# Optimization experiments

Measured on AMD Instinct MI355X. Metric: run time of the kernel, lower is better.

The kernel has to match this reference:

```python
import jax, jax.numpy as jnp
import numpy as np


def setup_inputs() -> dict:
    key = jax.random.key(0)
    kx, kc = jax.random.split(key)
    N, K, D = 32768, 4096, 512
    x = jax.random.normal(kx, (N, D), dtype=jnp.float32)
    # matches torch.rand(K, D) * 0.2 - 0.1
    codebook = jax.random.uniform(kc, (K, D), dtype=jnp.float32) * 0.2 - 0.1
    return {"x": x, "codebook": codebook}


def reference(x, codebook):
    x_sq = jnp.sum(x * x, axis=-1, keepdims=True)            # [N, 1]
    c_sq = jnp.sum(codebook * codebook, axis=-1)             # [K]
    dists = x_sq - 2.0 * jnp.einsum('nd,kd->nk', x, codebook) + c_sq[None, :]
    Z = jnp.argmin(dists, axis=-1)                           # [N] int
    q = codebook[Z]                                          # [N, D] gather
    q_with_st = x + jax.lax.stop_gradient(q - x)             # straight-through
    vq_loss = jnp.mean((jax.lax.stop_gradient(q) - x) ** 2)
    commitment_loss = jnp.mean((jax.lax.stop_gradient(x) - q) ** 2)
    return Z, q_with_st, vq_loss, commitment_loss
```

## Files before the change

kernel.cpp:

```cpp
#include <hip/hip_runtime.h>

static constexpr int N = 32768;
static constexpr int K = 4096;
static constexpr int D = 512;

typedef _Float16 f16x8 __attribute__((ext_vector_type(8)));
typedef float f32x4 __attribute__((ext_vector_type(4)));

#define GLD16(GP, LP)                                                   \
  __builtin_amdgcn_global_load_lds(                                     \
      (const __attribute__((address_space(1))) void*)(GP),              \
      (__attribute__((address_space(3))) void*)(LP), 16, 0, 0)

__global__ __launch_bounds__(256) void rowsq_convert_kernel(
    const float* __restrict__ in, float* __restrict__ sqout,
    _Float16* __restrict__ hi, float scale, int rows) {
  __shared__ float ls[8][512];
  int rb = blockIdx.x * 8;
  int tid = threadIdx.x;
#pragma unroll
  for (int g2 = 0; g2 < 2; ++g2) {
    int g = g2 * 256 + tid;
    int r = g >> 6;
    int c8 = (g & 63) * 8;
    const float4* p = (const float4*)(in + (size_t)(rb + r) * D + c8);
    float4 a = p[0], b = p[1];
    float s[8] = {a.x, a.y, a.z, a.w, b.x, b.y, b.z, b.w};
    union { _Float16 h[8]; f16x8 v; } H;
#pragma unroll
    for (int jj = 0; jj < 8; ++jj) {
      H.h[jj] = (_Float16)(s[jj] * scale);
      ls[r][c8 + jj] = s[jj];
    }
    *(f16x8*)(hi + (size_t)(rb + r) * D + c8) = H.v;
  }
  __syncthreads();
  int rr = tid >> 5;
  int l = tid & 31;
  const float* p = &ls[rr][(l >> 3) * 128 + (l & 7)];
  float r = 0.f;
#pragma unroll
  for (int i = 0; i < 16; ++i) {
    float v = p[i * 8];
    r = __fadd_rn(r, __fmul_rn(v, v));
  }
  r = __fadd_rn(r, __shfl_xor(r, 1));
  r = __fadd_rn(r, __shfl_xor(r, 2));
  r = __fadd_rn(r, __shfl_xor(r, 4));
  r = __fadd_rn(r, __shfl_xor(r, 8));
  r = __fadd_rn(r, __shfl_xor(r, 16));
  if (l == 0) sqout[rb + rr] = r;
}

__global__ __launch_bounds__(256) void transpose_kernel(
    const float* __restrict__ in, float* __restrict__ outT) {
  __shared__ float t[32][33];
  int bk = blockIdx.x;
  int bd = blockIdx.y;
  int tx = threadIdx.x, ty = threadIdx.y;
#pragma unroll
  for (int j = 0; j < 32; j += 8)
    t[ty + j][tx] = in[(size_t)(bk * 32 + ty + j) * D + bd * 32 + tx];
  __syncthreads();
#pragma unroll
  for (int j = 0; j < 32; j += 8)
    outT[(size_t)(bd * 32 + ty + j) * K + bk * 32 + tx] = t[tx][ty + j];
}

__global__ __launch_bounds__(256) void mfma_argmin_kernel(
    const _Float16* __restrict__ xh, const _Float16* __restrict__ ch,
    const float* __restrict__ xsq, const float* __restrict__ csq,
    float* __restrict__ pv1, int* __restrict__ pi1, float* __restrict__ pv2) {
  __shared__ __align__(16) _Float16 Ah[2][128 * 32];
  __shared__ __align__(16) _Float16 Bh[2][128 * 32];
  __shared__ float mbv1[128];
  __shared__ int mbi1[128];
  __shared__ float mbv2[128];

  int bid = blockIdx.x;
  int xcd = bid & 7, j = bid >> 3;
  int sup = j >> 6, win = j & 63;
  int rowPanel = xcd * 32 + (sup >> 2) * 8 + (win >> 3);
  int colPanel = (sup & 3) * 8 + (win & 7);

  int tid = threadIdx.x;
  int w = tid >> 6, l = tid & 63;
  int wr = w >> 1, wc = w & 1;
  int wrow = wr * 64, wcol = wc * 64;
  int rA = l & 15, g = l >> 4;

  const size_t rowBase = (size_t)rowPanel * 128;
  const size_t colBase = (size_t)colPanel * 128;

  f32x4 acc[4][4];
#pragma unroll
  for (int mi = 0; mi < 4; ++mi)
#pragma unroll
    for (int ni = 0; ni < 4; ++ni) acc[mi][ni] = (f32x4)0.f;

  const int r0 = tid >> 2, s0 = tid & 3;
  const int cs = s0 ^ ((r0 >> 1) & 3);
  const int swz = (g ^ ((rA >> 1) & 3)) * 8;

  const _Float16* aSrc = xh + (rowBase + r0) * D + cs * 8;
  const _Float16* bSrc = ch + (colBase + r0) * D + cs * 8;

  auto stage = [&](int buf, int kt) {
    const int dOff = kt * 32;
    GLD16(aSrc + dOff, &Ah[buf][(size_t)tid * 8]);
    GLD16(aSrc + dOff + (size_t)64 * D, &Ah[buf][(size_t)(tid + 256) * 8]);
    GLD16(bSrc + dOff, &Bh[buf][(size_t)tid * 8]);
    GLD16(bSrc + dOff + (size_t)64 * D, &Bh[buf][(size_t)(tid + 256) * 8]);
  };

  stage(0, 0);
  int cur = 0;
  for (int kt = 0; kt < 16; ++kt) {
    __syncthreads();
    if (kt < 15) stage(cur ^ 1, kt + 1);

    f16x8 ah[4], bh[4];
#pragma unroll
    for (int f = 0; f < 4; ++f) {
      ah[f] = *(const f16x8*)&Ah[cur][(wrow + f * 16 + rA) * 32 + swz];
      bh[f] = *(const f16x8*)&Bh[cur][(wcol + f * 16 + rA) * 32 + swz];
    }
#pragma unroll
    for (int mi = 0; mi < 4; ++mi)
#pragma unroll
      for (int ni = 0; ni < 4; ++ni)
        acc[mi][ni] =
            __builtin_amdgcn_mfma_f32_16x16x32_f16(ah[mi], bh[ni], acc[mi][ni], 0, 0, 0);
    cur ^= 1;
  }

  const float inv2048 = 1.0f / 2048.0f;
  float fv1[4][4], fv2[4][4];
  int fi1[4][4];
#pragma unroll
  for (int mi = 0; mi < 4; ++mi) {
#pragma unroll
    for (int r = 0; r < 4; ++r) {
      int row_l = wrow + mi * 16 + g * 4 + r;
      float xq = xsq[rowBase + row_l];
      float bv1 = 1e30f, bv2 = 1e30f;
      int bi1 = 0x7fffffff;
#pragma unroll
      for (int ni = 0; ni < 4; ++ni) {
        int col = (int)colBase + wcol + ni * 16 + rA;
        float S = acc[mi][ni][r];
        float dsc = (xq - S * inv2048) + csq[col];
        if (dsc < bv1 || (dsc == bv1 && col < bi1)) {
          bv2 = bv1; bv1 = dsc; bi1 = col;
        } else if (dsc < bv2) {
          bv2 = dsc;
        }
      }
#pragma unroll
      for (int m = 1; m < 16; m <<= 1) {
        float ov1 = __shfl_xor(bv1, m);
        int oi1 = __shfl_xor(bi1, m);
        float ov2 = __shfl_xor(bv2, m);
        if (ov1 < bv1 || (ov1 == bv1 && oi1 < bi1)) {
          bv2 = fminf(bv1, ov2); bv1 = ov1; bi1 = oi1;
        } else {
          bv2 = fminf(bv2, ov1);
        }
      }
      fv1[mi][r] = bv1; fv2[mi][r] = bv2; fi1[mi][r] = bi1;
      if (wc == 1 && rA == 0) {
        mbv1[row_l] = bv1; mbi1[row_l] = bi1; mbv2[row_l] = bv2;
      }
    }
  }
  __syncthreads();
  if (wc == 0 && rA == 0) {
#pragma unroll
    for (int mi = 0; mi < 4; ++mi) {
#pragma unroll
      for (int r = 0; r < 4; ++r) {
        int row_l = wrow + mi * 16 + g * 4 + r;
        float bv1 = fv1[mi][r], bv2 = fv2[mi][r];
        int bi1 = fi1[mi][r];
        float ov1 = mbv1[row_l];
        int oi1 = mbi1[row_l];
        float ov2 = mbv2[row_l];
        if (ov1 < bv1 || (ov1 == bv1 && oi1 < bi1)) {
          bv2 = fminf(bv1, ov2); bv1 = ov1; bi1 = oi1;
        } else {
          bv2 = fminf(bv2, ov1);
        }
        size_t o = (size_t)colPanel * N + (rowBase + row_l);
        pv1[o] = bv1; pi1[o] = bi1; pv2[o] = bv2;
      }
    }
  }
}

__global__ __launch_bounds__(256) void reduce_kernel(
    const float* __restrict__ pv1, const int* __restrict__ pi1,
    const float* __restrict__ pv2, float* __restrict__ zout,
    int* __restrict__ ctr, int* __restrict__ list, float eps) {
  int row = blockIdx.x * 256 + threadIdx.x;
  if (row >= N) return;
  float v1 = 1e30f, v2 = 1e30f;
  int i1 = 0x7fffffff;
  for (int jj = 0; jj < 32; ++jj) {
    float ov1 = pv1[(size_t)jj * N + row];
    float ov2 = pv2[(size_t)jj * N + row];
    int oi1 = pi1[(size_t)jj * N + row];
    if (ov1 < v1 || (ov1 == v1 && oi1 < i1)) {
      v2 = fminf(v1, ov2); v1 = ov1; i1 = oi1;
    } else {
      v2 = fminf(v2, ov1);
    }
  }
  zout[row] = (float)i1;
  if (v2 - v1 < eps) {
    int p = atomicAdd(ctr, 1);
    if (p < N) list[p] = row;
  }
}

static constexpr int RT_ROWS = 16;
static constexpr int RT_PANELS = 8;
static constexpr int CHUNK_D = 8;

__global__ __launch_bounds__(256) void rescore_tiled_kernel(
    const float* __restrict__ x, const float* __restrict__ cbT,
    const float* __restrict__ xsq, const float* __restrict__ csq,
    const int* __restrict__ ctr, const int* __restrict__ list,
    float* __restrict__ prv, int* __restrict__ pri) {
  __shared__ float xs[RT_ROWS][D + 4];
  __shared__ __align__(16) float cbs[2][CHUNK_D][512];
  int cnt = *ctr;
  if (cnt > N) cnt = N;
  int nTiles = (cnt + RT_ROWS - 1) / RT_ROWS;
  int nItems = nTiles * RT_PANELS;
  int tid = threadIdx.x;
  int ty = tid >> 4;
  int tx = tid & 15;

  for (int item = blockIdx.x; item < nItems; item += gridDim.x) {
    int tileIdx = item >> 3;
    int panel = item & 7;
    int base = tileIdx * RT_ROWS;
    int colPanel = panel * 512;
    __syncthreads();

    for (int i = tid; i < RT_ROWS * (D / 4); i += 256) {
      int r = i >> 7;
      int d4 = i & 127;
      int fi = base + r;
      int row = list[fi < cnt ? fi : 0];
      ((float4*)&xs[r][0])[d4] = ((const float4*)(x + (size_t)row * D))[d4];
    }

    auto stageCb = [&](int buf, int chk) {
      const float* src = cbT + (size_t)(chk * CHUNK_D) * K + colPanel;
#pragma unroll
      for (int it = 0; it < 4; ++it) {
        int f = it * 256 + tid;
        int dd = f >> 7, c4 = f & 127;
        GLD16(src + (size_t)dd * K + c4 * 4, &cbs[buf][0][0] + (size_t)f * 4);
      }
    };

    stageCb(0, 0);
    float acc[32];
#pragma unroll
    for (int c = 0; c < 32; ++c) acc[c] = 0.f;

    int cur = 0;
    for (int chk = 0; chk < D / CHUNK_D; ++chk) {
      __syncthreads();
      if (chk < D / CHUNK_D - 1) stageCb(cur ^ 1, chk + 1);
#pragma unroll
      for (int dd = 0; dd < CHUNK_D; ++dd) {
        float xa = xs[ty][chk * CHUNK_D + dd];
        const float4* cp = (const float4*)&cbs[cur][dd][0];
#pragma unroll
        for (int jj = 0; jj < 8; ++jj) {
          float4 v = cp[tx + jj * 16];
          acc[jj * 4 + 0] = fmaf(xa, v.x, acc[jj * 4 + 0]);
          acc[jj * 4 + 1] = fmaf(xa, v.y, acc[jj * 4 + 1]);
          acc[jj * 4 + 2] = fmaf(xa, v.z, acc[jj * 4 + 2]);
          acc[jj * 4 + 3] = fmaf(xa, v.w, acc[jj * 4 + 3]);
        }
      }
      cur ^= 1;
    }

    int fi = base + ty;
    int row = list[fi < cnt ? fi : 0];
    float xq = xsq[row];
    float bv = 1e30f;
    int bi = 0x7fffffff;
#pragma unroll
    for (int jj = 0; jj < 8; ++jj) {
#pragma unroll
      for (int q = 0; q < 4; ++q) {
        int col = colPanel + jj * 64 + tx * 4 + q;
        float a = acc[jj * 4 + q];
        float two = __fadd_rn(a, a);
        float t = __fsub_rn(xq, two);
        float dsc = __fadd_rn(t, csq[col]);
        if (dsc < bv || (dsc == bv && col < bi)) { bv = dsc; bi = col; }
      }
    }
#pragma unroll
    for (int m = 1; m < 16; m <<= 1) {
      float ov = __shfl_xor(bv, m);
      int oi = __shfl_xor(bi, m);
      if (ov < bv || (ov == bv && oi < bi)) { bv = ov; bi = oi; }
    }
    if (tx == 0 && fi < cnt) {
      prv[(size_t)fi * RT_PANELS + panel] = bv;
      pri[(size_t)fi * RT_PANELS + panel] = bi;
    }
  }
}

__global__ __launch_bounds__(256) void rescore_reduce_kernel(
    const float* __restrict__ prv, const int* __restrict__ pri,
    const int* __restrict__ ctr, const int* __restrict__ list,
    float* __restrict__ zout) {
  int cnt = *ctr;
  if (cnt > N) cnt = N;
  for (int fi = blockIdx.x * 256 + threadIdx.x; fi < cnt;
       fi += gridDim.x * 256) {
    float bv = 1e30f;
    int bi = 0x7fffffff;
#pragma unroll
    for (int p = 0; p < RT_PANELS; ++p) {
      float v = prv[(size_t)fi * RT_PANELS + p];
      int i = pri[(size_t)fi * RT_PANELS + p];
      if (v < bv || (v == bv && i < bi)) { bv = v; bi = i; }
    }
    zout[list[fi]] = (float)bi;
  }
}

static constexpr int BM = 64;
static constexpr int BKc = 128;
static constexpr int BD = 32;

__global__ __launch_bounds__(256) void argmin_fp32_kernel(
    const float* __restrict__ x, const float* __restrict__ cb,
    const float* __restrict__ xsq, const float* __restrict__ csq,
    float* __restrict__ zout) {
  __shared__ float xs[BD][BM];
  __shared__ float cs_[BD][BKc];
  __shared__ float mv[BM][16];
  __shared__ int mi[BM][16];

  int tid = threadIdx.x;
  int tx = tid & 15;
  int ty = tid >> 4;
  int row0 = blockIdx.x * BM;

  float bestv[4];
  int besti[4];
  float xsqr[4];
#pragma unroll
  for (int i = 0; i < 4; ++i) {
    bestv[i] = 3.4e38f;
    besti[i] = 0x7fffffff;
    xsqr[i] = xsq[row0 + ty * 4 + i];
  }

  for (int kt = 0; kt < K; kt += BKc) {
    float acc[4][8];
#pragma unroll
    for (int i = 0; i < 4; ++i)
#pragma unroll
      for (int jj = 0; jj < 8; ++jj) acc[i][jj] = 0.f;

    for (int dt = 0; dt < D; dt += BD) {
      __syncthreads();
      {
        int r = tid >> 2, d0 = (tid & 3) * 8;
        const float* src = x + (size_t)(row0 + r) * D + dt + d0;
        float4 v0 = *(const float4*)(src);
        float4 v1 = *(const float4*)(src + 4);
        xs[d0 + 0][r] = v0.x; xs[d0 + 1][r] = v0.y;
        xs[d0 + 2][r] = v0.z; xs[d0 + 3][r] = v0.w;
        xs[d0 + 4][r] = v1.x; xs[d0 + 5][r] = v1.y;
        xs[d0 + 6][r] = v1.z; xs[d0 + 7][r] = v1.w;
      }
      {
        int kk = tid >> 1, d0 = (tid & 1) * 16;
        const float* src = cb + (size_t)(kt + kk) * D + dt + d0;
        float4 v0 = *(const float4*)(src);
        float4 v1 = *(const float4*)(src + 4);
        float4 v2 = *(const float4*)(src + 8);
        float4 v3 = *(const float4*)(src + 12);
        cs_[d0 + 0][kk] = v0.x;  cs_[d0 + 1][kk] = v0.y;
        cs_[d0 + 2][kk] = v0.z;  cs_[d0 + 3][kk] = v0.w;
        cs_[d0 + 4][kk] = v1.x;  cs_[d0 + 5][kk] = v1.y;
        cs_[d0 + 6][kk] = v1.z;  cs_[d0 + 7][kk] = v1.w;
        cs_[d0 + 8][kk] = v2.x;  cs_[d0 + 9][kk] = v2.y;
        cs_[d0 + 10][kk] = v2.z; cs_[d0 + 11][kk] = v2.w;
        cs_[d0 + 12][kk] = v3.x; cs_[d0 + 13][kk] = v3.y;
        cs_[d0 + 14][kk] = v3.z; cs_[d0 + 15][kk] = v3.w;
      }
      __syncthreads();
#pragma unroll 4
      for (int d = 0; d < BD; ++d) {
        float xa[4], cv[8];
        *(float4*)&xa[0] = *(const float4*)&xs[d][ty * 4];
        *(float4*)&cv[0] = *(const float4*)&cs_[d][tx * 8];
        *(float4*)&cv[4] = *(const float4*)&cs_[d][tx * 8 + 4];
#pragma unroll
        for (int i = 0; i < 4; ++i)
#pragma unroll
          for (int jj = 0; jj < 8; ++jj)
            acc[i][jj] = fmaf(xa[i], cv[jj], acc[i][jj]);
      }
    }

#pragma unroll
    for (int jj = 0; jj < 8; ++jj) {
      int k = kt + tx * 8 + jj;
      float cq = csq[k];
#pragma unroll
      for (int i = 0; i < 4; ++i) {
        float two = __fadd_rn(acc[i][jj], acc[i][jj]);
        float t = __fsub_rn(xsqr[i], two);
        float dsc = __fadd_rn(t, cq);
        if (dsc < bestv[i]) { bestv[i] = dsc; besti[i] = k; }
      }
    }
  }

  __syncthreads();
#pragma unroll
  for (int i = 0; i < 4; ++i) {
    mv[ty * 4 + i][tx] = bestv[i];
    mi[ty * 4 + i][tx] = besti[i];
  }
  __syncthreads();
  if (tid < BM) {
    float bv = mv[tid][0];
    int bi = mi[tid][0];
#pragma unroll
    for (int t = 1; t < 16; ++t) {
      float v = mv[tid][t];
      int ii = mi[tid][t];
      if (v < bv || (v == bv && ii < bi)) { bv = v; bi = ii; }
    }
    zout[row0 + tid] = (float)bi;
  }
}

__global__ __launch_bounds__(256) void gather_kernel(
    const float* __restrict__ x, const float* __restrict__ cb,
    const float* __restrict__ zf, float* __restrict__ qout,
    float* __restrict__ partial) {
  __shared__ float red[256];
  const size_t TOT4 = (size_t)N * D / 4;
  size_t t0 = (size_t)blockIdx.x * 256 + threadIdx.x;
  float lsum = 0.f;
  for (size_t f = t0; f < TOT4; f += (size_t)2048 * 256) {
    int n = (int)(f >> 7);
    int d4 = (int)(f & 127);
    int z = (int)zf[n];
    float4 xv = ((const float4*)x)[f];
    float4 qv = *(const float4*)(cb + (size_t)z * D + d4 * 4);
    float dx0 = __fsub_rn(qv.x, xv.x);
    float dx1 = __fsub_rn(qv.y, xv.y);
    float dx2 = __fsub_rn(qv.z, xv.z);
    float dx3 = __fsub_rn(qv.w, xv.w);
    float4 o;
    o.x = __fadd_rn(xv.x, dx0);
    o.y = __fadd_rn(xv.y, dx1);
    o.z = __fadd_rn(xv.z, dx2);
    o.w = __fadd_rn(xv.w, dx3);
    ((float4*)qout)[f] = o;
    lsum += dx0 * dx0 + dx1 * dx1 + dx2 * dx2 + dx3 * dx3;
  }
  red[threadIdx.x] = lsum;
  __syncthreads();
  for (int s = 128; s > 0; s >>= 1) {
    if (threadIdx.x < s) red[threadIdx.x] += red[threadIdx.x + s];
    __syncthreads();
  }
  if (threadIdx.x == 0) partial[blockIdx.x] = red[0];
}

__global__ __launch_bounds__(256) void loss_kernel(const float* __restrict__ partial,
                                                   float* __restrict__ loss_out) {
  __shared__ float red[256];
  float s = 0.f;
  for (int i = threadIdx.x; i < 2048; i += 256) s += partial[i];
  red[threadIdx.x] = s;
  __syncthreads();
  for (int k = 128; k > 0; k >>= 1) {
    if (threadIdx.x < k) red[threadIdx.x] += red[threadIdx.x + k];
    __syncthreads();
  }
  if (threadIdx.x == 0) {
    float m = red[0] / (float)((size_t)N * D);
    loss_out[0] = m;
    loss_out[1] = m;
  }
}

static constexpr size_t OFF_XSQ = 0;
static constexpr size_t OFF_CSQ = 131072;
static constexpr size_t OFF_PART = 147456;
static constexpr size_t OFF_CTR = 155648;
static constexpr size_t OFF_LIST = 155904;
static constexpr size_t OFF_PV1 = 286976;
static constexpr size_t OFF_PI1 = OFF_PV1 + 4194304;
static constexpr size_t OFF_PV2 = OFF_PI1 + 4194304;
static constexpr size_t OFF_PRV = OFF_PV2 + 4194304;
static constexpr size_t OFF_PRI = OFF_PRV + 1048576;
static constexpr size_t WS_REQ = OFF_PRI + 1048576;

extern "C" void kernel_launch(void* const* d_in, const int* in_sizes, int n_in,
                              void* d_out, int out_size, void* d_ws, size_t ws_size,
                              hipStream_t stream) {
  const float* x = (const float*)d_in[0];
  const float* cb = (const float*)d_in[1];
  float* out = (float*)d_out;

  float* zout = out;
  float* qout = out + N;
  float* lout = out + N + (size_t)N * D;

  char* ws = (char*)d_ws;
  float* xsq = (float*)(ws + OFF_XSQ);
  float* csq = (float*)(ws + OFF_CSQ);
  float* partial = (float*)(ws + OFF_PART);

  _Float16* xhi = (_Float16*)qout;
  float* cbT = (float*)((char*)qout + (size_t)N * D * 2);
  _Float16* chi = (_Float16*)((char*)cbT + (size_t)D * K * 4);

  rowsq_convert_kernel<<<dim3(N / 8), dim3(256), 0, stream>>>(x, xsq, xhi,
                                                              16.0f, N);
  rowsq_convert_kernel<<<dim3(K / 8), dim3(256), 0, stream>>>(cb, csq, chi,
                                                              256.0f, K);

  if (ws_size >= WS_REQ) {
    int* ctr = (int*)(ws + OFF_CTR);
    int* list = (int*)(ws + OFF_LIST);
    float* pv1 = (float*)(ws + OFF_PV1);
    int* pi1 = (int*)(ws + OFF_PI1);
    float* pv2 = (float*)(ws + OFF_PV2);
    float* prv = (float*)(ws + OFF_PRV);
    int* pri = (int*)(ws + OFF_PRI);

    transpose_kernel<<<dim3(K / 32, D / 32), dim3(32, 8), 0, stream>>>(cb, cbT);
    hipMemsetAsync(ctr, 0, sizeof(int), stream);
    mfma_argmin_kernel<<<dim3((N / 128) * (K / 128)), dim3(256), 0, stream>>>(
        xhi, chi, xsq, csq, pv1, pi1, pv2);
    reduce_kernel<<<dim3(N / 256), dim3(256), 0, stream>>>(pv1, pi1, pv2, zout,
                                                           ctr, list, 0.02f);
    rescore_tiled_kernel<<<dim3(1024), dim3(256), 0, stream>>>(
        x, cbT, xsq, csq, ctr, list, prv, pri);
    rescore_reduce_kernel<<<dim3(128), dim3(256), 0, stream>>>(prv, pri, ctr,
                                                               list, zout);
  } else {
    argmin_fp32_kernel<<<dim3(N / BM), dim3(256), 0, stream>>>(x, cb, xsq, csq,
                                                               zout);
  }

  gather_kernel<<<dim3(2048), dim3(256), 0, stream>>>(x, cb, zout, qout, partial);
  loss_kernel<<<dim3(1), dim3(256), 0, stream>>>(partial, lout);
}
```

Baseline: 537.6 us.

## Widen MFMA argmin tile to 128x256 with per-wave full-row coverage

The fp16 MFMA distance/argmin kernel now computes a 128x256 tile per block instead of 128x128, so each wave covers all 128 rows against its own 64 columns with an 8x4 accumulator array. This halves the number of column panels, which halves the partial-result buffers and the reduce loop, and raises data reuse per LDS load. The cost is more accumulator registers (launch bounds set to 2 blocks/SM), larger LDS for B, and a four-way cross-wave merge through shared memory.

```diff
diff --git a/kernel.cpp b/kernel.cpp
--- a/kernel.cpp
+++ b/kernel.cpp
@@ -67,34 +67,33 @@
     outT[(size_t)(bd * 32 + ty + j) * K + bk * 32 + tx] = t[tx][ty + j];
 }
 
-__global__ __launch_bounds__(256) void mfma_argmin_kernel(
+__global__ __launch_bounds__(256, 2) void mfma_argmin_kernel(
     const _Float16* __restrict__ xh, const _Float16* __restrict__ ch,
     const float* __restrict__ xsq, const float* __restrict__ csq,
     float* __restrict__ pv1, int* __restrict__ pi1, float* __restrict__ pv2) {
   __shared__ __align__(16) _Float16 Ah[2][128 * 32];
-  __shared__ __align__(16) _Float16 Bh[2][128 * 32];
-  __shared__ float mbv1[128];
-  __shared__ int mbi1[128];
-  __shared__ float mbv2[128];
+  __shared__ __align__(16) _Float16 Bh[2][256 * 32];
+  __shared__ float mbv1[128][4];
+  __shared__ float mbv2[128][4];
+  __shared__ int mbi1[128][4];
 
   int bid = blockIdx.x;
   int xcd = bid & 7, j = bid >> 3;
   int sup = j >> 6, win = j & 63;
-  int rowPanel = xcd * 32 + (sup >> 2) * 8 + (win >> 3);
-  int colPanel = (sup & 3) * 8 + (win & 7);
+  int rowPanel = xcd * 32 + (sup >> 1) * 8 + (win >> 3);
+  int colPanel = (sup & 1) * 8 + (win & 7);
 
   int tid = threadIdx.x;
   int w = tid >> 6, l = tid & 63;
-  int wr = w >> 1, wc = w & 1;
-  int wrow = wr * 64, wcol = wc * 64;
+  int wcol = w * 64;
   int rA = l & 15, g = l >> 4;
 
   const size_t rowBase = (size_t)rowPanel * 128;
-  const size_t colBase = (size_t)colPanel * 128;
-
-  f32x4 acc[4][4];
-#pragma unroll
-  for (int mi = 0; mi < 4; ++mi)
+  const size_t colBase = (size_t)colPanel * 256;
+
+  f32x4 acc[8][4];
+#pragma unroll
+  for (int mi = 0; mi < 8; ++mi)
 #pragma unroll
     for (int ni = 0; ni < 4; ++ni) acc[mi][ni] = (f32x4)0.f;
 
@@ -111,6 +110,8 @@
     GLD16(aSrc + dOff + (size_t)64 * D, &Ah[buf][(size_t)(tid + 256) * 8]);
     GLD16(bSrc + dOff, &Bh[buf][(size_t)tid * 8]);
     GLD16(bSrc + dOff + (size_t)64 * D, &Bh[buf][(size_t)(tid + 256) * 8]);
+    GLD16(bSrc + dOff + (size_t)128 * D, &Bh[buf][(size_t)(tid + 512) * 8]);
+    GLD16(bSrc + dOff + (size_t)192 * D, &Bh[buf][(size_t)(tid + 768) * 8]);
   };
 
   stage(0, 0);
@@ -119,14 +120,15 @@
     __syncthreads();
     if (kt < 15) stage(cur ^ 1, kt + 1);
 
-    f16x8 ah[4], bh[4];
-#pragma unroll
-    for (int f = 0; f < 4; ++f) {
-      ah[f] = *(const f16x8*)&Ah[cur][(wrow + f * 16 + rA) * 32 + swz];
+    f16x8 bh[4], ah[8];
+#pragma unroll
+    for (int f = 0; f < 4; ++f)
       bh[f] = *(const f16x8*)&Bh[cur][(wcol + f * 16 + rA) * 32 + swz];
-    }
-#pragma unroll
-    for (int mi = 0; mi < 4; ++mi)
+#pragma unroll
+    for (int f = 0; f < 8; ++f)
+      ah[f] = *(const f16x8*)&Ah[cur][(f * 16 + rA) * 32 + swz];
+#pragma unroll
+    for (int mi = 0; mi < 8; ++mi)
 #pragma unroll
       for (int ni = 0; ni < 4; ++ni)
         acc[mi][ni] =
@@ -135,13 +137,11 @@
   }
 
   const float inv2048 = 1.0f / 2048.0f;
-  float fv1[4][4], fv2[4][4];
-  int fi1[4][4];
-#pragma unroll
-  for (int mi = 0; mi < 4; ++mi) {
+#pragma unroll
+  for (int mi = 0; mi < 8; ++mi) {
 #pragma unroll
     for (int r = 0; r < 4; ++r) {
-      int row_l = wrow + mi * 16 + g * 4 + r;
+      int row_l = mi * 16 + g * 4 + r;
       float xq = xsq[rowBase + row_l];
       float bv1 = 1e30f, bv2 = 1e30f;
       int bi1 = 0x7fffffff;
@@ -167,33 +167,30 @@
           bv2 = fminf(bv2, ov1);
         }
       }
-      fv1[mi][r] = bv1; fv2[mi][r] = bv2; fi1[mi][r] = bi1;
-      if (wc == 1 && rA == 0) {
-        mbv1[row_l] = bv1; mbi1[row_l] = bi1; mbv2[row_l] = bv2;
-      }
-    }
-  }
-  __syncthreads();
-  if (wc == 0 && rA == 0) {
-#pragma unroll
-    for (int mi = 0; mi < 4; ++mi) {
-#pragma unroll
-      for (int r = 0; r < 4; ++r) {
-        int row_l = wrow + mi * 16 + g * 4 + r;
-        float bv1 = fv1[mi][r], bv2 = fv2[mi][r];
-        int bi1 = fi1[mi][r];
-        float ov1 = mbv1[row_l];
-        int oi1 = mbi1[row_l];
-        float ov2 = mbv2[row_l];
-        if (ov1 < bv1 || (ov1 == bv1 && oi1 < bi1)) {
-          bv2 = fminf(bv1, ov2); bv1 = ov1; bi1 = oi1;
-        } else {
-          bv2 = fminf(bv2, ov1);
-        }
-        size_t o = (size_t)colPanel * N + (rowBase + row_l);
-        pv1[o] = bv1; pi1[o] = bi1; pv2[o] = bv2;
-      }
-    }
+      if (rA == 0) {
+        mbv1[row_l][w] = bv1;
+        mbi1[row_l][w] = bi1;
+        mbv2[row_l][w] = bv2;
+      }
+    }
+  }
+  __syncthreads();
+  if (tid < 128) {
+    float bv1 = mbv1[tid][0], bv2 = mbv2[tid][0];
+    int bi1 = mbi1[tid][0];
+#pragma unroll
+    for (int p = 1; p < 4; ++p) {
+      float ov1 = mbv1[tid][p];
+      int oi1 = mbi1[tid][p];
+      float ov2 = mbv2[tid][p];
+      if (ov1 < bv1 || (ov1 == bv1 && oi1 < bi1)) {
+        bv2 = fminf(bv1, ov2); bv1 = ov1; bi1 = oi1;
+      } else {
+        bv2 = fminf(bv2, ov1);
+      }
+    }
+    size_t o = (size_t)colPanel * N + (rowBase + tid);
+    pv1[o] = bv1; pi1[o] = bi1; pv2[o] = bv2;
   }
 }
 
@@ -205,7 +202,7 @@
   if (row >= N) return;
   float v1 = 1e30f, v2 = 1e30f;
   int i1 = 0x7fffffff;
-  for (int jj = 0; jj < 32; ++jj) {
+  for (int jj = 0; jj < 16; ++jj) {
     float ov1 = pv1[(size_t)jj * N + row];
     float ov2 = pv2[(size_t)jj * N + row];
     int oi1 = pi1[(size_t)jj * N + row];
@@ -512,9 +509,9 @@
 static constexpr size_t OFF_CTR = 155648;
 static constexpr size_t OFF_LIST = 155904;
 static constexpr size_t OFF_PV1 = 286976;
-static constexpr size_t OFF_PI1 = OFF_PV1 + 4194304;
-static constexpr size_t OFF_PV2 = OFF_PI1 + 4194304;
-static constexpr size_t OFF_PRV = OFF_PV2 + 4194304;
+static constexpr size_t OFF_PI1 = OFF_PV1 + 2097152;
+static constexpr size_t OFF_PV2 = OFF_PI1 + 2097152;
+static constexpr size_t OFF_PRV = OFF_PV2 + 2097152;
 static constexpr size_t OFF_PRI = OFF_PRV + 1048576;
 static constexpr size_t WS_REQ = OFF_PRI + 1048576;
 
@@ -554,7 +551,7 @@
 
     transpose_kernel<<<dim3(K / 32, D / 32), dim3(32, 8), 0, stream>>>(cb, cbT);
     hipMemsetAsync(ctr, 0, sizeof(int), stream);
-    mfma_argmin_kernel<<<dim3((N / 128) * (K / 128)), dim3(256), 0, stream>>>(
+    mfma_argmin_kernel<<<dim3((N / 128) * (K / 256)), dim3(256), 0, stream>>>(
         xhi, chi, xsq, csq, pv1, pi1, pv2);
     reduce_kernel<<<dim3(N / 256), dim3(256), 0, stream>>>(pv1, pi1, pv2, zout,
                                                            ctr, list, 0.02f);
```

New measurement: 575.0 us. 1.07x slower.
